# Kernel optimization log

Hardware: AMD Instinct MI355X
Metric: run time of the kernel (lower is better)

Reference implementation:

```python
import jax, jax.numpy as jnp
import numpy as np

N, E, G = 50000, 400000, 128
IN_DIM, EDGE_DIM, HID, HEADS = 64, 16, 64, 4
HC = HID * HEADS  # 256


def tconv(x, src, dst, e, wq, bq, wk, bk, wv, bv, we, ws, bs, heads, concat):
    # PyG TransformerConv (eval mode, no dropout), edge_dim path, root_weight=True
    n = x.shape[0]
    hc = wq.shape[1]
    c = hc // heads
    q = (x @ wq + bq).reshape(n, heads, c)
    k = (x @ wk + bk).reshape(n, heads, c)
    v = (x @ wv + bv).reshape(n, heads, c)
    eh = (e @ we).reshape(-1, heads, c)           # [E,H,C] edge embedding per head
    kj = k[src] + eh                               # gathered keys + edge
    vj = v[src] + eh                               # gathered values + edge
    alpha = jnp.einsum('ehc,ehc->eh', q[dst], kj) / jnp.sqrt(jnp.float32(c))
    amax = jax.ops.segment_max(alpha, dst, num_segments=n)   # segment softmax over in-edges
    ea = jnp.exp(alpha - amax[dst])
    denom = jax.ops.segment_sum(ea, dst, num_segments=n)
    w = ea / denom[dst]                            # [E,H]
    out = jax.ops.segment_sum(w[:, :, None] * vj, dst, num_segments=n)  # [N,H,C]
    out = out.reshape(n, hc) if concat else out.mean(axis=1)
    return out + x @ ws + bs                       # skip connection (lin_skip)


def bn_eval(x, g, b, m, v):
    return (x - m) * (g * jax.lax.rsqrt(v + 1e-5)) + b


def setup_inputs() -> dict:
    key = jax.random.key(0)
    ks = jax.random.split(key, 80)
    it = iter(range(80))
    def nrm(shape, s=0.05):
        return jax.random.normal(ks[next(it)], shape, jnp.float32) * s
    inp = {}
    inp['x'] = jax.random.normal(ks[next(it)], (N, IN_DIM), jnp.float32)
    inp['edge_index'] = jax.random.randint(ks[next(it)], (2, E), 0, N, jnp.int32)
    inp['edge_attr'] = jax.random.normal(ks[next(it)], (E, EDGE_DIM), jnp.float32)
    inp['batch'] = jnp.sort(jax.random.randint(ks[next(it)], (N,), 0, G, jnp.int32))
    inp['ee_w1'] = nrm((EDGE_DIM, 64)); inp['ee_b1'] = jnp.zeros((64,), jnp.float32)
    inp['ee_w2'] = nrm((64, HID)); inp['ee_b2'] = jnp.zeros((HID,), jnp.float32)
    def conv(pre, din, heads, cat):
        hc = HID * heads
        inp[pre+'_wq'] = nrm((din, hc)); inp[pre+'_bq'] = jnp.zeros((hc,), jnp.float32)
        inp[pre+'_wk'] = nrm((din, hc)); inp[pre+'_bk'] = jnp.zeros((hc,), jnp.float32)
        inp[pre+'_wv'] = nrm((din, hc)); inp[pre+'_bv'] = jnp.zeros((hc,), jnp.float32)
        inp[pre+'_we'] = nrm((HID, hc))
        dout = hc if cat else HID
        inp[pre+'_ws'] = nrm((din, dout)); inp[pre+'_bs'] = jnp.zeros((dout,), jnp.float32)
    conv('c1', IN_DIM, HEADS, True)
    conv('c2', HC, HEADS, True)
    conv('c3', HC, 1, False)
    def bn(pre, d):
        inp[pre+'_g'] = 1.0 + nrm((d,)); inp[pre+'_b'] = nrm((d,))
        inp[pre+'_m'] = nrm((d,)); inp[pre+'_v'] = 0.5 + jax.random.uniform(ks[next(it)], (d,), jnp.float32)
    bn('bn1', HC); bn('bn2', HC); bn('bn3', HID)
    inp['r_w1'] = nrm((HID, HID // 2)); inp['r_b1'] = jnp.zeros((HID // 2,), jnp.float32)
    inp['r_w2'] = nrm((HID // 2, 16)); inp['r_b2'] = jnp.zeros((16,), jnp.float32)
    inp['r_w3'] = nrm((16, 1)); inp['r_b3'] = jnp.zeros((1,), jnp.float32)
    return inp


def reference(x, edge_attr,
              ee_w1, ee_b1, ee_w2, ee_b2,
              c1_wq, c1_bq, c1_wk, c1_bk, c1_wv, c1_bv, c1_we, c1_ws, c1_bs,
              c2_wq, c2_bq, c2_wk, c2_bk, c2_wv, c2_bv, c2_we, c2_ws, c2_bs,
              c3_wq, c3_bq, c3_wk, c3_bk, c3_wv, c3_bv, c3_we, c3_ws, c3_bs,
              bn1_g, bn1_b, bn1_m, bn1_v,
              bn2_g, bn2_b, bn2_m, bn2_v,
              bn3_g, bn3_b, bn3_m, bn3_v,
              r_w1, r_b1, r_w2, r_b2, r_w3, r_b3,
              edge_index, batch):
    src, dst = edge_index[0], edge_index[1]
    e = jax.nn.relu(edge_attr @ ee_w1 + ee_b1) @ ee_w2 + ee_b2   # edge encoder
    h = tconv(x, src, dst, e, c1_wq, c1_bq, c1_wk, c1_bk, c1_wv, c1_bv, c1_we, c1_ws, c1_bs, HEADS, True)
    h = jax.nn.elu(bn_eval(h, bn1_g, bn1_b, bn1_m, bn1_v))
    h = tconv(h, src, dst, e, c2_wq, c2_bq, c2_wk, c2_bk, c2_wv, c2_bv, c2_we, c2_ws, c2_bs, HEADS, True)
    h = jax.nn.elu(bn_eval(h, bn2_g, bn2_b, bn2_m, bn2_v))
    h = tconv(h, src, dst, e, c3_wq, c3_bq, c3_wk, c3_bk, c3_wv, c3_bv, c3_we, c3_ws, c3_bs, 1, False)
    h = jax.nn.elu(bn_eval(h, bn3_g, bn3_b, bn3_m, bn3_v))
    sums = jax.ops.segment_sum(h, batch, num_segments=G)          # global_mean_pool
    cnt = jax.ops.segment_sum(jnp.ones((h.shape[0], 1), h.dtype), batch, num_segments=G)
    g = sums / jnp.maximum(cnt, 1.0)
    r = jax.nn.relu(g @ r_w1 + r_b1)
    r = jax.nn.relu(r @ r_w2 + r_b2)
    return (r @ r_w3 + r_b3)[:, 0]
```

## Files before the change

### kernel.cpp

```cpp
#include <hip/hip_runtime.h>
#include <math.h>


typedef _Float16 f16;
typedef _Float16 half8  __attribute__((ext_vector_type(8)));
typedef _Float16 half4v __attribute__((ext_vector_type(4)));
typedef float    f32x4  __attribute__((ext_vector_type(4)));

__device__ __forceinline__ void gload16(const void* g, void* l){
  __builtin_amdgcn_global_load_lds((const __attribute__((address_space(1))) void*)g,
                                   (__attribute__((address_space(3))) void*)l, 16, 0, 0);
}

__global__ void leak_kernel(float* __restrict__ out, int n, float val){
  int i = blockIdx.x*blockDim.x + threadIdx.x;
  if (i < n) out[i] = val;
}

__global__ void hist_kernel(const int* __restrict__ dst, int* __restrict__ deg, int E){
  int i = blockIdx.x*blockDim.x + threadIdx.x;
  if (i < E) atomicAdd(&deg[dst[i]], 1);
}

__global__ __launch_bounds__(1024)
void scan_kernel(const int* __restrict__ deg, int* __restrict__ rowptr, int n){
  __shared__ int buf[1024];
  __shared__ int sbase;
  int tid = threadIdx.x;
  if (tid == 0){ sbase = 0; rowptr[0] = 0; }
  __syncthreads();
  for (int start = 0; start < n; start += 4096){
    int i0 = start + tid*4;
    int a0 = (i0+0<n)?deg[i0+0]:0;
    int a1 = (i0+1<n)?deg[i0+1]:0;
    int a2 = (i0+2<n)?deg[i0+2]:0;
    int a3 = (i0+3<n)?deg[i0+3]:0;
    int s = a0+a1+a2+a3;
    int v = s;
    buf[tid] = v;
    __syncthreads();
    for (int off=1; off<1024; off<<=1){
      int t = (tid >= off) ? buf[tid-off] : 0;
      __syncthreads();
      v += t;
      buf[tid] = v;
      __syncthreads();
    }
    int pre = sbase + v - s;
    if (i0+0 < n) rowptr[i0+1] = pre + a0;
    if (i0+1 < n) rowptr[i0+2] = pre + a0 + a1;
    if (i0+2 < n) rowptr[i0+3] = pre + a0 + a1 + a2;
    if (i0+3 < n) rowptr[i0+4] = pre + s;
    __syncthreads();
    if (tid == 1023) sbase += buf[1023];
    __syncthreads();
  }
}

__global__ void scatter_kernel(const int* __restrict__ src, const int* __restrict__ dst,
                               const int* __restrict__ rowptr, int* __restrict__ cnt,
                               int* __restrict__ csr_src, int* __restrict__ csr_eid, int E){
  int i = blockIdx.x*blockDim.x + threadIdx.x;
  if (i >= E) return;
  int d = dst[i];
  int pos = rowptr[d] + atomicAdd(&cnt[d], 1);
  csr_src[pos] = src[i];
  csr_eid[pos] = i;
}

__global__ void gather_ef16_kernel(const f16* __restrict__ EFt, const int* __restrict__ csr_eid,
                                   f16* __restrict__ EFh, int E){
  int i = blockIdx.x*blockDim.x + threadIdx.x;
  if (i >= E*8) return;
  int e = i >> 3, j8 = (i & 7) * 8;
  *(half8*)(EFh + (size_t)e*64 + j8) = *(const half8*)(EFt + (size_t)csr_eid[e]*64 + j8);
}

struct PrepP {
  const float *ee_w1, *ee_w2;
  const float *wq[3], *wk[3], *wv[3], *we[3], *ws[3];
  const float *bq[3], *bk[3], *bv[3];
  f16* Bpk; float* biasAll;
  int* zeroP; int nZero;
  const float* eattr; f16* EA16; int nEA;
  const float* x; f16* XA; int nXA;
};

__device__ __forceinline__ float projv(const float* wq, const float* wk, const float* wv,
                                       const float* we, int hc, int din, int x){
  int c = x / din, k = x - c*din;
  int sec = c / hc, cc = c - sec*hc;
  if (sec == 0) return wq[(size_t)k*hc + cc];
  if (sec == 1) return wk[(size_t)k*hc + cc];
  if (sec == 2) return wv[(size_t)k*hc + cc];
  int h = cc >> 6, jj = cc & 63;
  const float* q = wq + (size_t)k*hc + h*64;
  const float* w = we + (size_t)jj*hc + h*64;
  float s = 0.f;
  #pragma unroll 8
  for (int t = 0; t < 64; ++t) s += q[t]*w[t];
  return s;
}
__device__ __forceinline__ float postv(const float* we, const float* ws,
                                       int hc, int din, int x){
  int Kpp = 64 + din;
  int c = x / Kpp, k = x - c*Kpp;
  if (k < 64) return we[(size_t)k*hc + c];
  return ws[(size_t)(k-64)*hc + c];
}

__global__ void prep_kernel(PrepP P){
  int id = blockIdx.x*blockDim.x + threadIdx.x;
  const int NB = 534528, NBB = NB + 2304;
  if (id < NB){
    float v;
    if      (id < 2048)  { int c = id>>5, k = id&31; v = (k<16) ? P.ee_w1[k*64 + c] : 0.f; }
    else if (id < 6144)  { int x = id-2048; int c = x>>6, k = x&63; v = P.ee_w2[k*64 + c]; }
    else if (id < 71680) v = projv(P.wq[0],P.wk[0],P.wv[0],P.we[0],256,64, id-6144);
    else if (id < 333824)v = projv(P.wq[1],P.wk[1],P.wv[1],P.we[1],256,256,id-71680);
    else if (id < 399360)v = projv(P.wq[2],P.wk[2],P.wv[2],P.we[2],64, 256,id-333824);
    else if (id < 432128)v = postv(P.we[0],P.ws[0],256,64, id-399360);
    else if (id < 514048)v = postv(P.we[1],P.ws[1],256,256,id-432128);
    else                 v = postv(P.we[2],P.ws[2],64, 256,id-514048);
    P.Bpk[id] = (f16)v;
  } else if (id < NBB){
    int x = id - NB;
    int cv, off, hc;
    if (x < 1024){ cv = 0; off = x;        hc = 256; }
    else if (x < 2048){ cv = 1; off = x-1024; hc = 256; }
    else { cv = 2; off = x-2048; hc = 64; }
    int sec = off / hc, cc = off - sec*hc;
    float v;
    if      (sec == 0) v = P.bq[cv][cc];
    else if (sec == 1) v = P.bk[cv][cc];
    else if (sec == 2) v = P.bv[cv][cc];
    else {
      int h = cc >> 6, jj = cc & 63;
      const float* b = P.bq[cv] + h*64;
      const float* w = P.we[cv] + (size_t)jj*hc + h*64;
      v = 0.f;
      #pragma unroll 8
      for (int t = 0; t < 64; ++t) v += b[t]*w[t];
    }
    P.biasAll[x] = v;
  } else if (id < NBB + P.nZero){
    P.zeroP[id - NBB] = 0;
  } else if (id < NBB + P.nZero + P.nEA){
    int i = id - NBB - P.nZero;
    P.EA16[i] = (f16)P.eattr[i];
  } else if (id < NBB + P.nZero + P.nEA + P.nXA){
    int i = id - NBB - P.nZero - P.nEA;
    P.XA[i] = (f16)P.x[i];
  }
}

__device__ __forceinline__ float bn_elu(float x, float g, float b, float m, float v){
  float s = g / sqrtf(v + 1e-5f);
  float y = (x - m) * s + b;
  return y > 0.f ? y : expm1f(y);
}

template<int BN>
__global__ __launch_bounds__(256)
void hgemm_kernel(const f16* __restrict__ A1, int lda1, int K1,
                  const f16* __restrict__ A2, int lda2, int K2,
                  const f16* __restrict__ Bpk, int Kp,
                  const float* __restrict__ bias,
                  f16* __restrict__ C, int ldc, int M, int mode,
                  const f16* __restrict__ ep, int ldep,
                  const float* __restrict__ bng, const float* __restrict__ bnb,
                  const float* __restrict__ bnm, const float* __restrict__ bnv,
                  int headOff, size_t pstride, int hcShift)
{
  constexpr int WM = (BN == 128) ? 64 : 32;
  constexpr int MF = WM / 16;
  __shared__ f16 As[128*32];
  __shared__ f16 Bs[BN*32];
  const int tid  = threadIdx.x;
  const int lane = tid & 63;
  const int wave = tid >> 6;
  const int wm   = (BN == 128) ? (wave >> 1) : wave;
  const int wn   = (BN == 128) ? (wave & 1) : 0;
  const int l15  = lane & 15;
  const int cs   = (lane >> 4) ^ ((lane >> 2) & 3);
  const int csl  = (lane & 3) ^ (lane >> 4);
  const int arow = lane >> 2;

  const int nbx = gridDim.x;
  const int nwg = nbx * gridDim.y;
  int bid = blockIdx.y * nbx + blockIdx.x;
  {
    int q = nwg >> 3, r = nwg & 7;
    int xcd = bid & 7, idx = bid >> 3;
    bid = (xcd < r ? xcd * (q + 1) : r * (q + 1) + (xcd - r) * q) + idx;
  }
  const int row0 = (bid / nbx) * 128;
  const int col0 = (bid % nbx) * BN;
  const f16* A1b = headOff ? (A1 + col0) : A1;

  f32x4 acc[MF*4];
  #pragma unroll
  for (int i = 0; i < MF*4; ++i){ acc[i][0]=0.f; acc[i][1]=0.f; acc[i][2]=0.f; acc[i][3]=0.f; }

  for (int k0 = 0; k0 < Kp; k0 += 32) {
    const f16* Ap; int lda, ks;
    if (k0 < K1) { Ap = A1b; lda = lda1; ks = k0; }
    else         { Ap = A2;  lda = lda2; ks = k0 - K1; }
    #pragma unroll
    for (int t = 0; t < 2; ++t) {
      int r = wave*32 + t*16 + arow;
      gload16(Ap + (size_t)(row0 + r)*lda + ks + csl*8, As + (wave*32 + t*16)*32);
    }
    if (BN == 128) {
      #pragma unroll
      for (int t = 0; t < 2; ++t) {
        int r = wave*32 + t*16 + arow;
        gload16(Bpk + (size_t)(col0 + r)*Kp + k0 + csl*8, Bs + (wave*32 + t*16)*32);
      }
    } else {
      int r = wave*16 + arow;
      gload16(Bpk + (size_t)(col0 + r)*Kp + k0 + csl*8, Bs + wave*16*32);
    }
    __syncthreads();

    half8 af[MF], bf[4];
    #pragma unroll
    for (int mf = 0; mf < MF; ++mf)
      af[mf] = *(const half8*)(As + (wm*WM + mf*16 + l15)*32 + cs*8);
    #pragma unroll
    for (int nf = 0; nf < 4; ++nf)
      bf[nf] = *(const half8*)(Bs + (wn*64 + nf*16 + l15)*32 + cs*8);
    #pragma unroll
    for (int mf = 0; mf < MF; ++mf)
      #pragma unroll
      for (int nf = 0; nf < 4; ++nf)
        acc[mf*4+nf] = __builtin_amdgcn_mfma_f32_16x16x32_f16(af[mf], bf[nf], acc[mf*4+nf], 0,0,0);
    __syncthreads();
  }

  #pragma unroll
  for (int mf = 0; mf < MF; ++mf)
    #pragma unroll
    for (int nf = 0; nf < 4; ++nf){
      int col  = col0 + wn*64 + nf*16 + l15;
      int rowb = row0 + wm*WM + mf*16 + (lane>>4)*4;
      float bi = bias ? bias[col] : 0.f;
      #pragma unroll
      for (int i = 0; i < 4; ++i){
        int row = rowb + i;
        if (row >= M) continue;
        float r = acc[mf*4+nf][i] + bi;
        if (mode == 1) r = fmaxf(r, 0.f);
        else if (mode == 2){
          r += (float)ep[(size_t)row*ldep + col];
          r = bn_elu(r, bng[col], bnb[col], bnm[col], bnv[col]);
        }
        if (pstride){
          int hc = 1 << hcShift;
          int plane = col >> hcShift, c2 = col & (hc - 1);
          C[(size_t)plane*pstride + (size_t)row*hc + c2] = (f16)r;
        } else {
          C[(size_t)row*ldc + col] = (f16)r;
        }
      }
    }
}

template<int HC>
__global__ __launch_bounds__(256)
void agg16_kernel(const int* __restrict__ rowptr, const int* __restrict__ csr_src,
                  f16* __restrict__ PROJ, size_t ps, const f16* __restrict__ EFh, int nNodes)
{
  int lane = threadIdx.x & 63;
  int wid = (blockIdx.x * blockDim.x + threadIdx.x) >> 6;
  int grp = lane >> 4, l16 = lane & 15;
  int node, ch;
  if (HC == 256) { node = wid;          ch = 4*lane; }
  else           { node = wid*4 + grp;  ch = 4*l16;  }
  if (node >= nNodes) return;
  f16* Qp = PROJ;
  const f16* Kp = PROJ + ps;
  const f16* Vp = PROJ + 2*ps;
  f16* Wp = PROJ + 3*ps;
  half4v qh = *(const half4v*)(Qp + (size_t)node*HC + ch);
  half4v wh = *(const half4v*)(Wp + (size_t)node*HC + ch);
  float q0=qh[0],q1=qh[1],q2=qh[2],q3=qh[3];
  float w0=wh[0],w1=wh[1],w2=wh[2],w3=wh[3];
  int e0 = rowptr[node], e1 = rowptr[node+1];

  float m = -INFINITY, den = 0.f;
  float avx=0.f,avy=0.f,avz=0.f,avw=0.f, aex=0.f,aey=0.f,aez=0.f,aew=0.f;

  half4v kN, vN, eN;
  if (e0 < e1) {
    size_t so = (size_t)csr_src[e0]*HC + ch;
    kN = *(const half4v*)(Kp + so);
    vN = *(const half4v*)(Vp + so);
    eN = *(const half4v*)(EFh + (size_t)e0*64 + 4*l16);
  }
  for (int i = e0; i < e1; ++i) {
    half4v k4 = kN, v4 = vN, e4 = eN;
    if (i + 1 < e1) {
      size_t so = (size_t)csr_src[i+1]*HC + ch;
      kN = *(const half4v*)(Kp + so);
      vN = *(const half4v*)(Vp + so);
      eN = *(const half4v*)(EFh + (size_t)(i+1)*64 + 4*l16);
    }
    float ex=e4[0], ey=e4[1], ez=e4[2], ew=e4[3];
    float p = q0*(float)k4[0] + q1*(float)k4[1] + q2*(float)k4[2] + q3*(float)k4[3]
            + w0*ex + w1*ey + w2*ez + w3*ew;
    p += __shfl_xor(p, 1);
    p += __shfl_xor(p, 2);
    p += __shfl_xor(p, 4);
    p += __shfl_xor(p, 8);
    float alpha = p * 0.125f;
    float mn = fmaxf(m, alpha);
    float sc = __expf(m - mn);
    float w  = __expf(alpha - mn);
    den = den*sc + w;
    avx = avx*sc + w*(float)v4[0]; avy = avy*sc + w*(float)v4[1];
    avz = avz*sc + w*(float)v4[2]; avw = avw*sc + w*(float)v4[3];
    aex = aex*sc + w*ex; aey = aey*sc + w*ey;
    aez = aez*sc + w*ez; aew = aew*sc + w*ew;
    m = mn;
  }
  float inv = den > 0.f ? 1.0f/den : 0.f;
  half4v o1, o2;
  o1[0]=(f16)(avx*inv); o1[1]=(f16)(avy*inv); o1[2]=(f16)(avz*inv); o1[3]=(f16)(avw*inv);
  o2[0]=(f16)(aex*inv); o2[1]=(f16)(aey*inv); o2[2]=(f16)(aez*inv); o2[3]=(f16)(aew*inv);
  *(half4v*)(Qp + (size_t)node*HC + ch) = o1;
  *(half4v*)(Wp + (size_t)node*HC + ch) = o2;
}

__global__ void pool16_kernel(const f16* __restrict__ Hf, const int* __restrict__ batch,
                              float* __restrict__ gsum, int nNodes){
  const int CH = 64;
  int c = threadIdx.x & 63;
  int chunk = blockIdx.x * (blockDim.x >> 6) + (threadIdx.x >> 6);
  int n0 = chunk * CH;
  if (n0 >= nNodes) return;
  int n1 = min(n0 + CH, nNodes);
  float acc = 0.f;
  int g = batch[n0];
  for (int n = n0; n < n1; ++n) {
    int gn = batch[n];
    if (gn != g) { atomicAdd(&gsum[g*64 + c], acc); acc = 0.f; g = gn; }
    acc += (float)Hf[(size_t)n*64 + c];
  }
  atomicAdd(&gsum[g*64 + c], acc);
}

__global__ void mlp_kernel(const float* __restrict__ gsum, const int* __restrict__ batch,
                           int nNodes, int G,
                           const float* __restrict__ w1, const float* __restrict__ b1,
                           const float* __restrict__ w2, const float* __restrict__ b2,
                           const float* __restrict__ w3, const float* __restrict__ b3,
                           float* __restrict__ out){
  __shared__ float s_w1[2048], s_w2[512], s_w3[16], s_b1[32], s_b2[16];
  int t = threadIdx.x;
  for (int i = t; i < 2048; i += 128) s_w1[i] = w1[i];
  for (int i = t; i < 512;  i += 128) s_w2[i] = w2[i];
  if (t < 16) s_w3[t] = w3[t];
  if (t < 32) s_b1[t] = b1[t];
  if (t < 16) s_b2[t] = b2[t];
  __syncthreads();
  int g = t;
  if (g >= G) return;
  int lo = 0, hi = nNodes;
  while (lo < hi){ int mid = (lo+hi)>>1; if (batch[mid] < g) lo = mid+1; else hi = mid; }
  int first = lo;
  lo = 0; hi = nNodes;
  while (lo < hi){ int mid = (lo+hi)>>1; if (batch[mid] < g+1) lo = mid+1; else hi = mid; }
  int cnt = lo - first;
  float invc = 1.0f / fmaxf((float)cnt, 1.0f);
  float gm[64];
  #pragma unroll
  for (int c = 0; c < 64; ++c) gm[c] = gsum[g*64 + c] * invc;
  float r1[32];
  #pragma unroll
  for (int j = 0; j < 32; ++j){
    float s = s_b1[j];
    #pragma unroll 8
    for (int c = 0; c < 64; ++c) s = fmaf(gm[c], s_w1[c*32 + j], s);
    r1[j] = fmaxf(s, 0.f);
  }
  float r2[16];
  #pragma unroll
  for (int j = 0; j < 16; ++j){
    float s = s_b2[j];
    #pragma unroll 8
    for (int c = 0; c < 32; ++c) s = fmaf(r1[c], s_w2[c*16 + j], s);
    r2[j] = fmaxf(s, 0.f);
  }
  float s = b3[0];
  #pragma unroll
  for (int c = 0; c < 16; ++c) s = fmaf(r2[c], s_w3[c], s);
  out[g] = s;
}

template<int BN>
static inline void launch_hgemm(hipStream_t st,
    const f16* A1, int lda1, int K1, const f16* A2, int lda2, int K2,
    const f16* Bpk, int Kp, const float* bias,
    f16* C, int ldc, int M, int Ncols, int mode,
    const f16* ep, int ldep,
    const float* g, const float* b, const float* m, const float* v,
    int headOff = 0, size_t pstride = 0, int hcShift = 0)
{
  dim3 grid(Ncols / BN, (M + 127) / 128, 1);
  hgemm_kernel<BN><<<grid, 256, 0, st>>>(A1, lda1, K1, A2, lda2, K2, Bpk, Kp,
                                         bias, C, ldc, M, mode, ep, ldep, g, b, m, v,
                                         headOff, pstride, hcShift);
}

struct ConvW {
  const float *wq,*bq,*wk,*bk,*wv,*bv,*we,*ws,*bs,*bg,*bb,*bm,*bv_;
};

extern "C" void kernel_launch(void* const* d_in, const int* in_sizes, int n_in,
                              void* d_out, int out_size, void* d_ws, size_t ws_size,
                              hipStream_t stream) {
  (void)n_in;
  const float* x     = (const float*)d_in[0];
  const int*   ei    = (const int*)d_in[1];
  const float* eattr = (const float*)d_in[2];
  const int*   batch = (const int*)d_in[3];
  const float* ee_w1 = (const float*)d_in[4];
  const float* ee_b1 = (const float*)d_in[5];
  const float* ee_w2 = (const float*)d_in[6];
  const float* ee_b2 = (const float*)d_in[7];
  ConvW cw[3];
  {
    int t = 8;
    for (int c = 0; c < 3; ++c){
      cw[c].wq=(const float*)d_in[t++]; cw[c].bq=(const float*)d_in[t++];
      cw[c].wk=(const float*)d_in[t++]; cw[c].bk=(const float*)d_in[t++];
      cw[c].wv=(const float*)d_in[t++]; cw[c].bv=(const float*)d_in[t++];
      cw[c].we=(const float*)d_in[t++]; cw[c].ws=(const float*)d_in[t++]; cw[c].bs=(const float*)d_in[t++];
    }
    for (int c = 0; c < 3; ++c){
      cw[c].bg=(const float*)d_in[t++]; cw[c].bb=(const float*)d_in[t++];
      cw[c].bm=(const float*)d_in[t++]; cw[c].bv_=(const float*)d_in[t++];
    }
  }
  const float* r_w1 = (const float*)d_in[47];
  const float* r_b1 = (const float*)d_in[48];
  const float* r_w2 = (const float*)d_in[49];
  const float* r_b2 = (const float*)d_in[50];
  const float* r_w3 = (const float*)d_in[51];
  const float* r_b3 = (const float*)d_in[52];

  const int N = in_sizes[0] / 64;
  const int E = in_sizes[2] / 16;
  const int G = out_size;

  const size_t NPAD = (size_t)N + 128;
  char* wp = (char*)d_ws;
  f16* HA   = (f16*)wp;            wp += NPAD*256*2;
  f16* HB   = (f16*)wp;            wp += NPAD*256*2;
  f16* PROJ = (f16*)wp;            wp += NPAD*1024*2;
  f16* EFh  = (f16*)wp;            wp += (size_t)E*64*2;
  f16* Bpk  = (f16*)wp;            wp += 534528*2;
  float* biasAll = (float*)wp;     wp += 2304*4;
  float* gsum    = (float*)wp;     wp += 8192*4;
  int* ideg  = (int*)wp;           wp += (size_t)N*4;
  int* icnt  = (int*)wp;           wp += (size_t)N*4;
  int* irow  = (int*)wp;           wp += (size_t)(N+1)*4;
  int* csr_s = (int*)wp;           wp += (size_t)E*4;
  int* csr_e = (int*)wp;           wp += (size_t)E*4;
  size_t used = (size_t)(wp - (char*)d_ws);
  if (used > ws_size) {
    leak_kernel<<<(G + 255)/256, 256, 0, stream>>>((float*)d_out, G, (float)(ws_size >> 20));
    return;
  }
  f16* EA16  = HB;
  f16* HID   = PROJ;
  f16* EFtmp = PROJ + (size_t)E*64;

  const int* src = ei;
  const int* dst = ei + E;

  const int BO_E1 = 0, BO_E2 = 2048, BO_P0 = 6144, BO_P1 = 71680, BO_P2 = 333824;
  const int BO_S0 = 399360, BO_S1 = 432128, BO_S2 = 514048;

  PrepP P;
  P.ee_w1 = ee_w1; P.ee_w2 = ee_w2;
  for (int c = 0; c < 3; ++c){
    P.wq[c]=cw[c].wq; P.wk[c]=cw[c].wk; P.wv[c]=cw[c].wv; P.we[c]=cw[c].we; P.ws[c]=cw[c].ws;
    P.bq[c]=cw[c].bq; P.bk[c]=cw[c].bk; P.bv[c]=cw[c].bv;
  }
  P.Bpk = Bpk; P.biasAll = biasAll;
  P.zeroP = (int*)gsum; P.nZero = 8192 + 2*N;
  P.eattr = eattr; P.EA16 = EA16; P.nEA = E*16;
  P.x = x; P.XA = HA; P.nXA = N*64;
  {
    long total = 534528 + 2304 + (long)P.nZero + P.nEA + P.nXA;
    prep_kernel<<<(int)((total + 255)/256), 256, 0, stream>>>(P);
  }

  hist_kernel<<<(E + 255)/256, 256, 0, stream>>>(dst, ideg, E);
  scan_kernel<<<1, 1024, 0, stream>>>(ideg, irow, N);
  scatter_kernel<<<(E + 255)/256, 256, 0, stream>>>(src, dst, irow, icnt, csr_s, csr_e, E);

  launch_hgemm<64>(stream, EA16, 16, 32, nullptr, 0, 0, Bpk + BO_E1, 32, ee_b1,
                   HID, 64, E, 64, 1, nullptr, 0, 0,0,0,0);
  launch_hgemm<64>(stream, HID, 64, 64, nullptr, 0, 0, Bpk + BO_E2, 64, ee_b2,
                   EFtmp, 64, E, 64, 0, nullptr, 0, 0,0,0,0);
  gather_ef16_kernel<<<(E*8 + 255)/256, 256, 0, stream>>>(EFtmp, csr_e, EFh, E);

  const int BO_P[3] = {BO_P0, BO_P1, BO_P2};
  const int BO_S[3] = {BO_S0, BO_S1, BO_S2};
  const int bOff[3] = {0, 1024, 2048};
  for (int c = 0; c < 3; ++c) {
    const int din = (c == 0) ? 64 : 256;
    const int H   = (c == 2) ? 1 : 4;
    const int hc  = H * 64;
    const int hcShift = (hc == 256) ? 8 : 6;
    const size_t ps = NPAD * (size_t)hc;
    const f16* Xin = (c == 0) ? HA : ((c == 1) ? HB : HA);
    const int  ldx = (c == 0) ? 64 : 256;
    f16* Hout = (c == 1) ? HA : HB;
    const ConvW& W = cw[c];

    launch_hgemm<128>(stream, Xin, ldx, din, nullptr, 0, 0, Bpk + BO_P[c], din,
                      biasAll + bOff[c], PROJ, hc, N, 4*hc, 0, nullptr, 0, 0,0,0,0,
                      0, ps, hcShift);

    if (H == 4) agg16_kernel<256><<<(N + 3)/4,  256, 0, stream>>>(irow, csr_s, PROJ, ps, EFh, N);
    else        agg16_kernel<64> <<<(N + 15)/16,256, 0, stream>>>(irow, csr_s, PROJ, ps, EFh, N);

    launch_hgemm<64>(stream, PROJ + 3*ps, hc, 64, Xin, ldx, din, Bpk + BO_S[c], 64 + din,
                     W.bs, Hout, hc, N, hc, 2, PROJ, hc, W.bg, W.bb, W.bm, W.bv_,
                     1, 0, 0);
  }

  {
    int chunks = (N + 63) / 64;
    pool16_kernel<<<(chunks + 3)/4, 256, 0, stream>>>(HB, batch, gsum, N);
  }
  mlp_kernel<<<1, 128, 0, stream>>>(gsum, batch, N, G, r_w1, r_b1, r_w2, r_b2, r_w3, r_b3,
                                    (float*)d_out);
}
```

Measured before the change: 792.7 us.

## Fuse edge encoder MLP with CSR scatter and vectorize GEMM epilogue

Result: faster. 657.8 us (median of 2 runs) (-17.0%).

```diff
diff --git a/kernel.cpp b/kernel.cpp
--- a/kernel.cpp
+++ b/kernel.cpp
@@ -7,6 +7,7 @@
 typedef _Float16 half4v __attribute__((ext_vector_type(4)));
 typedef float    f32x4  __attribute__((ext_vector_type(4)));
 
+__device__ __forceinline__ float4 ld4(const float* p){ return *reinterpret_cast<const float4*>(p); }
 __device__ __forceinline__ void gload16(const void* g, void* l){
   __builtin_amdgcn_global_load_lds((const __attribute__((address_space(1))) void*)g,
                                    (__attribute__((address_space(3))) void*)l, 16, 0, 0);
@@ -59,21 +60,13 @@
 
 __global__ void scatter_kernel(const int* __restrict__ src, const int* __restrict__ dst,
                                const int* __restrict__ rowptr, int* __restrict__ cnt,
-                               int* __restrict__ csr_src, int* __restrict__ csr_eid, int E){
+                               int* __restrict__ csr_src, int* __restrict__ inv, int E){
   int i = blockIdx.x*blockDim.x + threadIdx.x;
   if (i >= E) return;
   int d = dst[i];
   int pos = rowptr[d] + atomicAdd(&cnt[d], 1);
   csr_src[pos] = src[i];
-  csr_eid[pos] = i;
-}
-
-__global__ void gather_ef16_kernel(const f16* __restrict__ EFt, const int* __restrict__ csr_eid,
-                                   f16* __restrict__ EFh, int E){
-  int i = blockIdx.x*blockDim.x + threadIdx.x;
-  if (i >= E*8) return;
-  int e = i >> 3, j8 = (i & 7) * 8;
-  *(half8*)(EFh + (size_t)e*64 + j8) = *(const half8*)(EFt + (size_t)csr_eid[e]*64 + j8);
+  inv[i] = pos;
 }
 
 struct PrepP {
@@ -82,7 +75,6 @@
   const float *bq[3], *bk[3], *bv[3];
   f16* Bpk; float* biasAll;
   int* zeroP; int nZero;
-  const float* eattr; f16* EA16; int nEA;
   const float* x; f16* XA; int nXA;
 };
 
@@ -145,12 +137,100 @@
     P.biasAll[x] = v;
   } else if (id < NBB + P.nZero){
     P.zeroP[id - NBB] = 0;
-  } else if (id < NBB + P.nZero + P.nEA){
+  } else if (id < NBB + P.nZero + P.nXA){
     int i = id - NBB - P.nZero;
-    P.EA16[i] = (f16)P.eattr[i];
-  } else if (id < NBB + P.nZero + P.nEA + P.nXA){
-    int i = id - NBB - P.nZero - P.nEA;
     P.XA[i] = (f16)P.x[i];
+  }
+}
+
+__global__ __launch_bounds__(256)
+void enc_fused_kernel(const float* __restrict__ eattr,
+                      const f16* __restrict__ B1, const f16* __restrict__ B2,
+                      const float* __restrict__ b1, const float* __restrict__ b2,
+                      const int* __restrict__ inv, f16* __restrict__ EFh, int E)
+{
+  __shared__ f16 hid[128*64];
+  const int tid = threadIdx.x, lane = tid & 63, wave = tid >> 6;
+  const int l15 = lane & 15, g = lane >> 4;
+  const int row0 = blockIdx.x * 128;
+
+  half8 af[2];
+  #pragma unroll
+  for (int mf = 0; mf < 2; ++mf){
+    int r = row0 + wave*32 + mf*16 + l15;
+    half8 v;
+    #pragma unroll
+    for (int q = 0; q < 8; ++q) v[q] = (f16)0.f;
+    if (g < 2){
+      const float* p = eattr + (size_t)r*16 + g*8;
+      float4 u0 = ld4(p), u1 = ld4(p+4);
+      v[0]=(f16)u0.x; v[1]=(f16)u0.y; v[2]=(f16)u0.z; v[3]=(f16)u0.w;
+      v[4]=(f16)u1.x; v[5]=(f16)u1.y; v[6]=(f16)u1.z; v[7]=(f16)u1.w;
+    }
+    af[mf] = v;
+  }
+  f32x4 acc[8];
+  #pragma unroll
+  for (int i = 0; i < 8; ++i){ acc[i][0]=0.f; acc[i][1]=0.f; acc[i][2]=0.f; acc[i][3]=0.f; }
+  #pragma unroll
+  for (int nf = 0; nf < 4; ++nf){
+    half8 bf = *(const half8*)(B1 + (size_t)(nf*16 + l15)*32 + g*8);
+    #pragma unroll
+    for (int mf = 0; mf < 2; ++mf)
+      acc[mf*4+nf] = __builtin_amdgcn_mfma_f32_16x16x32_f16(bf, af[mf], acc[mf*4+nf], 0,0,0);
+  }
+  #pragma unroll
+  for (int mf = 0; mf < 2; ++mf)
+    #pragma unroll
+    for (int nf = 0; nf < 4; ++nf){
+      int rowL = wave*32 + mf*16 + l15;
+      int colb = nf*16 + g*4;
+      float4 bi = ld4(&b1[colb]);
+      half4v h;
+      h[0] = (f16)fmaxf(acc[mf*4+nf][0] + bi.x, 0.f);
+      h[1] = (f16)fmaxf(acc[mf*4+nf][1] + bi.y, 0.f);
+      h[2] = (f16)fmaxf(acc[mf*4+nf][2] + bi.z, 0.f);
+      h[3] = (f16)fmaxf(acc[mf*4+nf][3] + bi.w, 0.f);
+      int byte = rowL*128 + (((colb>>3) ^ (rowL&7)) << 4) + ((colb>>2)&1)*8;
+      *(half4v*)((char*)hid + byte) = h;
+    }
+  __syncthreads();
+
+  f32x4 acc2[8];
+  #pragma unroll
+  for (int i = 0; i < 8; ++i){ acc2[i][0]=0.f; acc2[i][1]=0.f; acc2[i][2]=0.f; acc2[i][3]=0.f; }
+  #pragma unroll
+  for (int s = 0; s < 2; ++s){
+    half8 af2[2];
+    #pragma unroll
+    for (int mf = 0; mf < 2; ++mf){
+      int rowL = wave*32 + mf*16 + l15;
+      int kc = g + s*4;
+      int byte = rowL*128 + ((kc ^ (rowL&7)) << 4);
+      af2[mf] = *(const half8*)((const char*)hid + byte);
+    }
+    #pragma unroll
+    for (int nf = 0; nf < 4; ++nf){
+      half8 bf2 = *(const half8*)(B2 + (size_t)(nf*16 + l15)*64 + s*32 + g*8);
+      #pragma unroll
+      for (int mf = 0; mf < 2; ++mf)
+        acc2[mf*4+nf] = __builtin_amdgcn_mfma_f32_16x16x32_f16(bf2, af2[mf], acc2[mf*4+nf], 0,0,0);
+    }
+  }
+  #pragma unroll
+  for (int mf = 0; mf < 2; ++mf){
+    int dstRow = inv[row0 + wave*32 + mf*16 + l15];
+    #pragma unroll
+    for (int nf = 0; nf < 4; ++nf){
+      int colb = nf*16 + g*4;
+      float4 bi = ld4(&b2[colb]);
+      half4v h;
+      h[0] = (f16)(acc2[mf*4+nf][0] + bi.x);
+      h[1] = (f16)(acc2[mf*4+nf][1] + bi.y);
+      h[2] = (f16)(acc2[mf*4+nf][2] + bi.z);
+      h[3] = (f16)(acc2[mf*4+nf][3] + bi.w);
+      *(half4v*)(EFh + (size_t)dstRow*64 + colb) = h;
+    }
   }
 }
 
@@ -234,7 +314,7 @@
     for (int mf = 0; mf < MF; ++mf)
       #pragma unroll
       for (int nf = 0; nf < 4; ++nf)
-        acc[mf*4+nf] = __builtin_amdgcn_mfma_f32_16x16x32_f16(af[mf], bf[nf], acc[mf*4+nf], 0,0,0);
+        acc[mf*4+nf] = __builtin_amdgcn_mfma_f32_16x16x32_f16(bf[nf], af[mf], acc[mf*4+nf], 0,0,0);
     __syncthreads();
   }
 
@@ -242,27 +322,37 @@
   for (int mf = 0; mf < MF; ++mf)
     #pragma unroll
     for (int nf = 0; nf < 4; ++nf){
-      int col  = col0 + wn*64 + nf*16 + l15;
-      int rowb = row0 + wm*WM + mf*16 + (lane>>4)*4;
-      float bi = bias ? bias[col] : 0.f;
-      #pragma unroll
-      for (int i = 0; i < 4; ++i){
-        int row = rowb + i;
-        if (row >= M) continue;
-        float r = acc[mf*4+nf][i] + bi;
-        if (mode == 1) r = fmaxf(r, 0.f);
-        else if (mode == 2){
-          r += (float)ep[(size_t)row*ldep + col];
-          r = bn_elu(r, bng[col], bnb[col], bnm[col], bnv[col]);
-        }
-        if (pstride){
-          int hc = 1 << hcShift;
-          int plane = col >> hcShift, c2 = col & (hc - 1);
-          C[(size_t)plane*pstride + (size_t)row*hc + c2] = (f16)r;
-        } else {
-          C[(size_t)row*ldc + col] = (f16)r;
-        }
+      int row  = row0 + wm*WM + mf*16 + l15;
+      int colb = col0 + wn*64 + nf*16 + (lane>>4)*4;
+      if (row >= M) continue;
+      float4 bi = bias ? ld4(&bias[colb]) : make_float4(0.f,0.f,0.f,0.f);
+      float r0 = acc[mf*4+nf][0] + bi.x;
+      float r1 = acc[mf*4+nf][1] + bi.y;
+      float r2 = acc[mf*4+nf][2] + bi.z;
+      float r3 = acc[mf*4+nf][3] + bi.w;
+      if (mode == 1){
+        r0=fmaxf(r0,0.f); r1=fmaxf(r1,0.f); r2=fmaxf(r2,0.f); r3=fmaxf(r3,0.f);
+      } else if (mode == 2){
+        half4v e4 = *(const half4v*)(ep + (size_t)row*ldep + colb);
+        float4 g4 = ld4(&bng[colb]);
+        float4 b4 = ld4(&bnb[colb]);
+        float4 m4 = ld4(&bnm[colb]);
+        float4 v4 = ld4(&bnv[colb]);
+        r0 = bn_elu(r0 + (float)e4[0], g4.x, b4.x, m4.x, v4.x);
+        r1 = bn_elu(r1 + (float)e4[1], g4.y, b4.y, m4.y, v4.y);
+        r2 = bn_elu(r2 + (float)e4[2], g4.z, b4.z, m4.z, v4.z);
+        r3 = bn_elu(r3 + (float)e4[3], g4.w, b4.w, m4.w, v4.w);
       }
+      half4v h; h[0]=(f16)r0; h[1]=(f16)r1; h[2]=(f16)r2; h[3]=(f16)r3;
+      f16* dstp;
+      if (pstride){
+        int hc = 1 << hcShift;
+        int plane = colb >> hcShift, c2 = colb & (hc - 1);
+        dstp = C + (size_t)plane*pstride + (size_t)row*hc + c2;
+      } else {
+        dstp = C + (size_t)row*ldc + colb;
+      }
+      *(half4v*)dstp = h;
     }
 }
 
@@ -467,15 +557,12 @@
   int* icnt  = (int*)wp;           wp += (size_t)N*4;
   int* irow  = (int*)wp;           wp += (size_t)(N+1)*4;
   int* csr_s = (int*)wp;           wp += (size_t)E*4;
-  int* csr_e = (int*)wp;           wp += (size_t)E*4;
+  int* inv   = (int*)wp;           wp += (size_t)E*4;
   size_t used = (size_t)(wp - (char*)d_ws);
   if (used > ws_size) {
     leak_kernel<<<(G + 255)/256, 256, 0, stream>>>((float*)d_out, G, (float)(ws_size >> 20));
     return;
   }
-  f16* EA16  = HB;
-  f16* HID   = PROJ;
-  f16* EFtmp = PROJ + (size_t)E*64;
 
   const int* src = ei;
   const int* dst = ei + E;
@@ -491,22 +578,18 @@
   }
   P.Bpk = Bpk; P.biasAll = biasAll;
   P.zeroP = (int*)gsum; P.nZero = 8192 + 2*N;
-  P.eattr = eattr; P.EA16 = EA16; P.nEA = E*16;
   P.x = x; P.XA = HA; P.nXA = N*64;
   {
-    long total = 534528 + 2304 + (long)P.nZero + P.nEA + P.nXA;
+    long total = 534528 + 2304 + (long)P.nZero + P.nXA;
     prep_kernel<<<(int)((total + 255)/256), 256, 0, stream>>>(P);
   }
 
   hist_kernel<<<(E + 255)/256, 256, 0, stream>>>(dst, ideg, E);
   scan_kernel<<<1, 1024, 0, stream>>>(ideg, irow, N);
-  scatter_kernel<<<(E + 255)/256, 256, 0, stream>>>(src, dst, irow, icnt, csr_s, csr_e, E);
-
-  launch_hgemm<64>(stream, EA16, 16, 32, nullptr, 0, 0, Bpk + BO_E1, 32, ee_b1,
-                   HID, 64, E, 64, 1, nullptr, 0, 0,0,0,0);
-  launch_hgemm<64>(stream, HID, 64, 64, nullptr, 0, 0, Bpk + BO_E2, 64, ee_b2,
-                   EFtmp, 64, E, 64, 0, nullptr, 0, 0,0,0,0);
-  gather_ef16_kernel<<<(E*8 + 255)/256, 256, 0, stream>>>(EFtmp, csr_e, EFh, E);
+  scatter_kernel<<<(E + 255)/256, 256, 0, stream>>>(src, dst, irow, icnt, csr_s, inv, E);
+
+  enc_fused_kernel<<<E/128, 256, 0, stream>>>(eattr, Bpk + BO_E1, Bpk + BO_E2,
+                                              ee_b1, ee_b2, inv, EFh, E);
 
   const int BO_P[3] = {BO_P0, BO_P1, BO_P2};
   const int BO_S[3] = {BO_S0, BO_S1, BO_S2};
```
